# Kernel tuning notes

Measured on AMD Instinct MI355X. Metric: run time of the kernel, lower is better.

The kernel has to match this reference:

```python
import jax, jax.numpy as jnp
import numpy as np

B, T, C, H = 4, 2048, 1024, 16


def setup_inputs() -> dict:
    key = jax.random.key(0)
    k1, k2, k3 = jax.random.split(key, 3)
    x = jax.random.normal(k1, (B, T, C), dtype=jnp.float32)
    W_qkv = jax.random.normal(k2, (C, 3 * C), dtype=jnp.float32) * 0.02
    W_proj = jax.random.normal(k3, (C, C), dtype=jnp.float32) * 0.02
    return {"x": x, "W_qkv": W_qkv, "W_proj": W_proj}


def reference(x, W_qkv, W_proj):
    Bc, Tc, Cc = x.shape
    D = Cc // H
    qkv = x @ W_qkv                          # [B,T,3C]
    k, q, v = jnp.split(qkv, 3, axis=-1)     # split order k,q,v as in source
    q = q.reshape(Bc, Tc, H, D)
    k = k.reshape(Bc, Tc, H, D)
    v = v.reshape(Bc, Tc, H, D)
    # NOTE: module scales by full C**-0.5, not head_dim**-0.5
    scale = jnp.asarray(Cc, x.dtype) ** -0.5
    wei = jnp.einsum("bqhd,bkhd->bhqk", q, k) * scale      # [B,H,T,T]
    causal = jnp.tril(jnp.ones((Tc, Tc), dtype=bool))
    wei = jnp.where(causal[None, None], wei, jnp.asarray(-jnp.inf, x.dtype))
    att = jax.nn.softmax(wei, axis=-1)
    out = jnp.einsum("bhqk,bkhd->bqhd", att, v).reshape(Bc, Tc, Cc)
    return out @ W_proj
```

## Files before the change

kernel.cpp:

```cpp
#include <hip/hip_runtime.h>
#include <hip/hip_bf16.h>

#define B_   4
#define T_   2048
#define C_   1024
#define H_   16
#define D_   64
#define NQKV 3072
#define M_   (B_*T_)

typedef __attribute__((ext_vector_type(8))) short bf16x8;
typedef __attribute__((ext_vector_type(4))) short bf16x4;
typedef __attribute__((ext_vector_type(4))) float f32x4;
typedef __hip_bfloat16 bf16;

__device__ inline short f2bs(float f) {
    bf16 h = __float2bfloat16(f);
    return *(short*)&h;
}

__device__ inline void async_ld16(const bf16* g, bf16* l) {
    __builtin_amdgcn_global_load_lds(
        (const __attribute__((address_space(1))) void*)g,
        (__attribute__((address_space(3))) void*)l, 16, 0, 0);
}

__global__ __launch_bounds__(256) void prep(const float* __restrict__ x,
                                            const float* __restrict__ Wqkv,
                                            const float* __restrict__ Wproj,
                                            bf16* __restrict__ xb,
                                            bf16* __restrict__ wqkv_t,
                                            bf16* __restrict__ wproj_t) {
    __shared__ short t[32][33];
    const int bid = blockIdx.x;
    if (bid < 4096) {
        const long i = ((long)bid * 256 + threadIdx.x) * 8;
        const float4 a = *(const float4*)(x + i);
        const float4 bq = *(const float4*)(x + i + 4);
        bf16x8 o;
        o[0] = f2bs(a.x); o[1] = f2bs(a.y); o[2] = f2bs(a.z); o[3] = f2bs(a.w);
        o[4] = f2bs(bq.x); o[5] = f2bs(bq.y); o[6] = f2bs(bq.z); o[7] = f2bs(bq.w);
        *(bf16x8*)(xb + i) = o;
        return;
    }
    const float* in;  bf16* out;  int R, Ccol, r0, c0;
    if (bid < 7168) {
        const int b2 = bid - 4096;
        in = Wqkv; out = wqkv_t; R = C_; Ccol = NQKV;
        c0 = (b2 % 96) * 32; r0 = (b2 / 96) * 32;
    } else {
        const int b3 = bid - 7168;
        in = Wproj; out = wproj_t; R = C_; Ccol = C_;
        c0 = (b3 % 32) * 32; r0 = (b3 / 32) * 32;
    }
    const int xx = threadIdx.x & 31, yy = threadIdx.x >> 5;
#pragma unroll
    for (int i = 0; i < 4; i++)
        t[yy + 8*i][xx] = f2bs(in[(long)(r0 + yy + 8*i) * Ccol + c0 + xx]);
    __syncthreads();
#pragma unroll
    for (int i = 0; i < 4; i++)
        ((short*)out)[(long)(c0 + yy + 8*i) * R + r0 + xx] = t[xx][yy + 8*i];
}

__global__ __launch_bounds__(256) void transpose_v(const bf16* __restrict__ in,
                                                   bf16* __restrict__ out) {
    __shared__ short t[32][33];
    const int x = threadIdx.x & 31, y = threadIdx.x >> 5;
    const int t0 = blockIdx.x * 32, d0 = blockIdx.y * 32;
    const long base = (long)blockIdx.z * T_ * D_;
#pragma unroll
    for (int i = 0; i < 4; i++)
        t[y + 8*i][x] = ((const short*)in)[base + (long)(t0 + y + 8*i) * D_ + d0 + x];
    __syncthreads();
#pragma unroll
    for (int i = 0; i < 4; i++)
        ((short*)out)[base + (long)(d0 + y + 8*i) * T_ + t0 + x] = t[x][y + 8*i];
}

template<int MODE>
__global__ __launch_bounds__(256) void gemm_bt(const bf16* __restrict__ A,
                                               const bf16* __restrict__ Bt,
                                               float* __restrict__ outp,
                                               bf16* __restrict__ qb,
                                               bf16* __restrict__ kb,
                                               bf16* __restrict__ vb,
                                               int K, int N) {
    __shared__ __align__(16) bf16 As[128 * 32];
    __shared__ __align__(16) bf16 Bs[128 * 32];
    const int tid  = threadIdx.x;
    const int w    = tid >> 6, lane = tid & 63;
    const int g    = lane >> 4, ln = lane & 15;
    const int m0   = blockIdx.y * 128, n0 = blockIdx.x * 128;
    const int wm   = w & 1, wn = w >> 1;
    const int srow = lane >> 2;
    const int scol = (lane & 3) * 8;

    f32x4 acc[4][4] = {};

    for (int k0 = 0; k0 < K; k0 += 32) {
#pragma unroll
        for (int i = 0; i < 2; i++) {
            const int r = w * 32 + i * 16 + srow;
            async_ld16(A  + (long)(m0 + r) * K + k0 + scol, &As[r * 32 + scol]);
            async_ld16(Bt + (long)(n0 + r) * K + k0 + scol, &Bs[r * 32 + scol]);
        }
        __syncthreads();

        bf16x8 af[4], bfr[4];
#pragma unroll
        for (int i = 0; i < 4; i++)
            af[i]  = *(const bf16x8*)&As[(wm * 64 + i * 16 + ln) * 32 + g * 8];
#pragma unroll
        for (int j = 0; j < 4; j++)
            bfr[j] = *(const bf16x8*)&Bs[(wn * 64 + j * 16 + ln) * 32 + g * 8];
#pragma unroll
        for (int i = 0; i < 4; i++)
#pragma unroll
            for (int j = 0; j < 4; j++)
                acc[i][j] = __builtin_amdgcn_mfma_f32_16x16x32_bf16(af[i], bfr[j], acc[i][j], 0, 0, 0);
        __syncthreads();
    }

#pragma unroll
    for (int i = 0; i < 4; i++) {
#pragma unroll
        for (int j = 0; j < 4; j++) {
#pragma unroll
            for (int r = 0; r < 4; r++) {
                const int row = m0 + wm * 64 + i * 16 + g * 4 + r;
                const int col = n0 + wn * 64 + j * 16 + ln;
                if (MODE == 1) {
                    outp[(long)row * N + col] = acc[i][j][r];
                } else {
                    const int b = row >> 11, t = row & (T_ - 1);
                    const int seg = col >> 10;
                    const int c = col & (C_ - 1), h = c >> 6, d = c & 63;
                    if (seg == 0)
                        kb[(((long)(b * H_ + h)) * T_ + t) * D_ + d] = __float2bfloat16(acc[i][j][r]);
                    else if (seg == 1)
                        qb[(((long)(b * H_ + h)) * T_ + t) * D_ + d] = __float2bfloat16(acc[i][j][r] * 0.03125f);
                    else
                        vb[(((long)(b * H_ + h)) * T_ + t) * D_ + d] = __float2bfloat16(acc[i][j][r]);
                }
            }
        }
    }
}

__device__ inline void subtile(const bf16x8& qf0, const bf16x8& qf1,
                               f32x4* o, f32x4& l,
                               const short* Ks, const short* Vs, short* myP,
                               int q0, int kbase, int h2, int w, int g, int ln,
                               const bf16x8& ones) {
    f32x4 s[4] = {};
#pragma unroll
    for (int kj = 0; kj < 4; kj++) {
        const int krow = h2 * 64 + kj * 16 + ln;
        const bf16x8 kf0 = *(const bf16x8*)&Ks[krow * 64 + ((0 + g) ^ (krow & 7)) * 8];
        s[kj] = __builtin_amdgcn_mfma_f32_16x16x32_bf16(qf0, kf0, s[kj], 0, 0, 0);
        const bf16x8 kf1 = *(const bf16x8*)&Ks[krow * 64 + ((4 + g) ^ (krow & 7)) * 8];
        s[kj] = __builtin_amdgcn_mfma_f32_16x16x32_bf16(qf1, kf1, s[kj], 0, 0, 0);
    }
    const int rowg = q0 + w * 16 + g * 4;
    if (kbase == q0) {
#pragma unroll
        for (int kj = 0; kj < 4; kj++) {
            const int key = kbase + kj * 16 + ln;
#pragma unroll
            for (int r = 0; r < 4; r++) {
                float p = __expf(s[kj][r]);
                p = (key <= rowg + r) ? p : 0.f;
                const int prow = g * 4 + r;
                const int pc8 = (kj * 2 + (ln >> 3)) ^ (prow & 7);
                myP[prow * 64 + pc8 * 8 + (ln & 7)] = f2bs(p);
            }
        }
    } else {
#pragma unroll
        for (int kj = 0; kj < 4; kj++) {
#pragma unroll
            for (int r = 0; r < 4; r++) {
                const int prow = g * 4 + r;
                const int pc8 = (kj * 2 + (ln >> 3)) ^ (prow & 7);
                myP[prow * 64 + pc8 * 8 + (ln & 7)] = f2bs(__expf(s[kj][r]));
            }
        }
    }
    asm volatile("s_waitcnt lgkmcnt(0)" ::: "memory");
    const bf16x8 pf0 = *(const bf16x8*)&myP[ln * 64 + ((0 + g) ^ (ln & 7)) * 8];
    const bf16x8 pf1 = *(const bf16x8*)&myP[ln * 64 + ((4 + g) ^ (ln & 7)) * 8];
    l = __builtin_amdgcn_mfma_f32_16x16x32_bf16(ones, pf0, l, 0, 0, 0);
    l = __builtin_amdgcn_mfma_f32_16x16x32_bf16(ones, pf1, l, 0, 0, 0);
#pragma unroll
    for (int nb = 0; nb < 4; nb++) {
        const int drow = nb * 16 + ln;
        const bf16x8 vf0 = *(const bf16x8*)&Vs[drow * 128 + ((h2 * 8 + 0 + g) ^ (drow & 7)) * 8];
        o[nb] = __builtin_amdgcn_mfma_f32_16x16x32_bf16(vf0, pf0, o[nb], 0, 0, 0);
        const bf16x8 vf1 = *(const bf16x8*)&Vs[drow * 128 + ((h2 * 8 + 4 + g) ^ (drow & 7)) * 8];
        o[nb] = __builtin_amdgcn_mfma_f32_16x16x32_bf16(vf1, pf1, o[nb], 0, 0, 0);
    }
}

__global__ __launch_bounds__(256, 4) void flash(const bf16* __restrict__ qb,
                                                const bf16* __restrict__ kb,
                                                const bf16* __restrict__ vbT,
                                                bf16* __restrict__ att) {
    __shared__ __align__(16) short Ks[128 * 64];
    __shared__ __align__(16) short Vs[64 * 128];
    __shared__ __align__(16) short Ps[4 * 16 * 64];
    const int tid = threadIdx.x, w = tid >> 6, lane = tid & 63;
    const int g = lane >> 4, ln = lane & 15;
    const int lin = blockIdx.x;
    const int bh = lin & 63, p = lin >> 6;
    const int b = bh >> 4, h = bh & 15;
    const int q0A = p * 64, q0B = (31 - p) * 64;

    const bf16* qpA = qb + ((long)bh * T_ + q0A + w * 16 + ln) * D_;
    const bf16* qpB = qb + ((long)bh * T_ + q0B + w * 16 + ln) * D_;
    const bf16x8 qfA0 = *(const bf16x8*)(qpA + g * 8);
    const bf16x8 qfA1 = *(const bf16x8*)(qpA + 32 + g * 8);
    const bf16x8 qfB0 = *(const bf16x8*)(qpB + g * 8);
    const bf16x8 qfB1 = *(const bf16x8*)(qpB + 32 + g * 8);

    bf16x8 ones;
#pragma unroll
    for (int i = 0; i < 8; i++) ones[i] = 0x3F80;

    f32x4 oA[4] = {}, oB[4] = {};
    f32x4 lA = {}, lB = {};
    short* myP = &Ps[w * 16 * 64];

    const int nstB = (q0B + 64 + 127) >> 7;
    for (int s = 0; s < nstB; s++) {
        const int k0 = s * 128;
        bf16x8 kr[4], vr[4];
#pragma unroll
        for (int i = 0; i < 4; i++) {
            const int cc = i * 256 + tid;
            kr[i] = *(const bf16x8*)&kb [((long)bh * T_ + k0 + (cc >> 3)) * D_ + (cc & 7) * 8];
            vr[i] = *(const bf16x8*)&vbT[((long)bh * D_ + (cc >> 4)) * T_ + k0 + (cc & 15) * 8];
        }
        __syncthreads();
#pragma unroll
        for (int i = 0; i < 4; i++) {
            const int cc = i * 256 + tid;
            const int key = cc >> 3, c8 = cc & 7;
            *(bf16x8*)&Ks[key * 64 + (c8 ^ (key & 7)) * 8] = kr[i];
            const int d = cc >> 4, c16 = cc & 15;
            *(bf16x8*)&Vs[d * 128 + (c16 ^ (d & 7)) * 8] = vr[i];
        }
        __syncthreads();

#pragma unroll
        for (int h2 = 0; h2 < 2; h2++) {
            const int kbase = k0 + h2 * 64;
            if (kbase <= q0A + 63)
                subtile(qfA0, qfA1, oA, lA, Ks, Vs, myP, q0A, kbase, h2, w, g, ln, ones);
            if (kbase <= q0B + 63)
                subtile(qfB0, qfB1, oB, lB, Ks, Vs, myP, q0B, kbase, h2, w, g, ln, ones);
        }
    }

#pragma unroll
    for (int ti = 0; ti < 2; ti++) {
        const f32x4* o = ti ? oB : oA;
        const float invl = 1.f / (ti ? lB[0] : lA[0]);
        const int q = (ti ? q0B : q0A) + w * 16 + ln;
#pragma unroll
        for (int nb = 0; nb < 4; nb++) {
            bf16x4 pk;
#pragma unroll
            for (int r = 0; r < 4; r++) pk[r] = f2bs(o[nb][r] * invl);
            *(bf16x4*)&att[((long)b * T_ + q) * C_ + h * D_ + nb * 16 + g * 4] = pk;
        }
    }
}

extern "C" void kernel_launch(void* const* d_in, const int* in_sizes, int n_in,
                              void* d_out, int out_size, void* d_ws, size_t ws_size,
                              hipStream_t stream) {
    const float* x     = (const float*)d_in[0];
    const float* Wqkv  = (const float*)d_in[1];
    const float* Wproj = (const float*)d_in[2];
    float* out = (float*)d_out;

    char* ws = (char*)d_ws;
    bf16* wqkv_t  = (bf16*)(ws);
    bf16* wproj_t = (bf16*)(ws + 6291456);
    bf16* qb      = (bf16*)(ws + 8388608);
    bf16* kb      = (bf16*)(ws + 25165824);
    bf16* vb0     = (bf16*)(ws + 41943040);
    bf16* xb      = (bf16*)(ws + 58720256);
    bf16* vbT     = xb;
    bf16* att     = vb0;
    (void)ws_size; (void)in_sizes; (void)n_in; (void)out_size;

    prep<<<dim3(8192), dim3(256), 0, stream>>>(x, Wqkv, Wproj, xb, wqkv_t, wproj_t);
    gemm_bt<0><<<dim3(NQKV / 128, M_ / 128), dim3(256), 0, stream>>>(
        xb, wqkv_t, (float*)nullptr, qb, kb, vb0, C_, NQKV);
    transpose_v<<<dim3(T_ / 32, D_ / 32, B_ * H_), dim3(256), 0, stream>>>(vb0, vbT);
    flash<<<dim3(1024), dim3(256), 0, stream>>>(qb, kb, vbT, att);
    gemm_bt<1><<<dim3(C_ / 128, M_ / 128), dim3(256), 0, stream>>>(
        att, wproj_t, out, (bf16*)nullptr, (bf16*)nullptr, (bf16*)nullptr, C_, C_);
}
```

Before: 279.1 us.

## Fuse V transpose into QKV GEMM epilogue and widen GEMM K-tile with swizzle

```diff
diff --git a/kernel.cpp b/kernel.cpp
--- a/kernel.cpp
+++ b/kernel.cpp
@@ -19,7 +19,7 @@
     return *(short*)&h;
 }
 
-__device__ inline void async_ld16(const bf16* g, bf16* l) {
+__device__ inline void async_ld16(const bf16* g, const short* l) {
     __builtin_amdgcn_global_load_lds(
         (const __attribute__((address_space(1))) void*)g,
         (__attribute__((address_space(3))) void*)l, 16, 0, 0);
@@ -63,63 +63,77 @@
         ((short*)out)[(long)(c0 + yy + 8*i) * R + r0 + xx] = t[xx][yy + 8*i];
 }
 
-__global__ __launch_bounds__(256) void transpose_v(const bf16* __restrict__ in,
-                                                   bf16* __restrict__ out) {
-    __shared__ short t[32][33];
-    const int x = threadIdx.x & 31, y = threadIdx.x >> 5;
-    const int t0 = blockIdx.x * 32, d0 = blockIdx.y * 32;
-    const long base = (long)blockIdx.z * T_ * D_;
-#pragma unroll
-    for (int i = 0; i < 4; i++)
-        t[y + 8*i][x] = ((const short*)in)[base + (long)(t0 + y + 8*i) * D_ + d0 + x];
-    __syncthreads();
-#pragma unroll
-    for (int i = 0; i < 4; i++)
-        ((short*)out)[base + (long)(d0 + y + 8*i) * T_ + t0 + x] = t[x][y + 8*i];
-}
-
 template<int MODE>
 __global__ __launch_bounds__(256) void gemm_bt(const bf16* __restrict__ A,
                                                const bf16* __restrict__ Bt,
                                                float* __restrict__ outp,
                                                bf16* __restrict__ qb,
                                                bf16* __restrict__ kb,
-                                               bf16* __restrict__ vb,
+                                               bf16* __restrict__ vbT,
                                                int K, int N) {
-    __shared__ __align__(16) bf16 As[128 * 32];
-    __shared__ __align__(16) bf16 Bs[128 * 32];
+    __shared__ __align__(16) short SMEM[18432];
+    short* As = SMEM;
+    short* Bs = SMEM + 8192;
     const int tid  = threadIdx.x;
     const int w    = tid >> 6, lane = tid & 63;
     const int g    = lane >> 4, ln = lane & 15;
     const int m0   = blockIdx.y * 128, n0 = blockIdx.x * 128;
     const int wm   = w & 1, wn = w >> 1;
-    const int srow = lane >> 2;
-    const int scol = (lane & 3) * 8;
 
     f32x4 acc[4][4] = {};
 
-    for (int k0 = 0; k0 < K; k0 += 32) {
-#pragma unroll
-        for (int i = 0; i < 2; i++) {
-            const int r = w * 32 + i * 16 + srow;
-            async_ld16(A  + (long)(m0 + r) * K + k0 + scol, &As[r * 32 + scol]);
-            async_ld16(Bt + (long)(n0 + r) * K + k0 + scol, &Bs[r * 32 + scol]);
-        }
-        __syncthreads();
-
-        bf16x8 af[4], bfr[4];
+    for (int k0 = 0; k0 < K; k0 += 64) {
+#pragma unroll
+        for (int i = 0; i < 4; i++) {
+            const int s   = w * 256 + i * 64 + lane;
+            const int row = s >> 3, c8 = (s & 7) ^ ((s >> 3) & 7);
+            async_ld16(A  + (long)(m0 + row) * K + k0 + c8 * 8, &As[s * 8]);
+            async_ld16(Bt + (long)(n0 + row) * K + k0 + c8 * 8, &Bs[s * 8]);
+        }
+        __syncthreads();
+
+#pragma unroll
+        for (int kh = 0; kh < 2; kh++) {
+            bf16x8 af[4], bfr[4];
+#pragma unroll
+            for (int i = 0; i < 4; i++)
+                af[i]  = *(const bf16x8*)&As[(wm * 64 + i * 16 + ln) * 64 + ((kh * 4 + g) ^ (ln & 7)) * 8];
+#pragma unroll
+            for (int j = 0; j < 4; j++)
+                bfr[j] = *(const bf16x8*)&Bs[(wn * 64 + j * 16 + ln) * 64 + ((kh * 4 + g) ^ (ln & 7)) * 8];
+#pragma unroll
+            for (int i = 0; i < 4; i++)
+#pragma unroll
+                for (int j = 0; j < 4; j++)
+                    acc[i][j] = __builtin_amdgcn_mfma_f32_16x16x32_bf16(af[i], bfr[j], acc[i][j], 0, 0, 0);
+        }
+        __syncthreads();
+    }
+
+    if (MODE == 0 && n0 >= 2048) {
+        short* Vt = SMEM;
 #pragma unroll
         for (int i = 0; i < 4; i++)
-            af[i]  = *(const bf16x8*)&As[(wm * 64 + i * 16 + ln) * 32 + g * 8];
-#pragma unroll
-        for (int j = 0; j < 4; j++)
-            bfr[j] = *(const bf16x8*)&Bs[(wn * 64 + j * 16 + ln) * 32 + g * 8];
-#pragma unroll
-        for (int i = 0; i < 4; i++)
 #pragma unroll
             for (int j = 0; j < 4; j++)
-                acc[i][j] = __builtin_amdgcn_mfma_f32_16x16x32_bf16(af[i], bfr[j], acc[i][j], 0, 0, 0);
-        __syncthreads();
+#pragma unroll
+                for (int r = 0; r < 4; r++) {
+                    const int tl = wm * 64 + i * 16 + g * 4 + r;
+                    const int dl = wn * 64 + j * 16 + ln;
+                    Vt[dl * 144 + tl] = f2bs(acc[i][j][r]);
+                }
+        __syncthreads();
+        const int b  = m0 >> 11, tb = m0 & (T_ - 1);
+        const int h0 = (n0 - 2048) >> 6;
+#pragma unroll
+        for (int ii = 0; ii < 8; ii++) {
+            const int s = ii * 256 + tid;
+            const int dl = s >> 4, t16 = s & 15;
+            const bf16x8 v = *(const bf16x8*)&Vt[dl * 144 + t16 * 8];
+            const int h = h0 + (dl >> 6), d = dl & 63;
+            *(bf16x8*)&vbT[(((long)(b * H_ + h)) * D_ + d) * T_ + tb + t16 * 8] = v;
+        }
+        return;
     }
 
 #pragma unroll
@@ -138,10 +152,8 @@
                     const int c = col & (C_ - 1), h = c >> 6, d = c & 63;
                     if (seg == 0)
                         kb[(((long)(b * H_ + h)) * T_ + t) * D_ + d] = __float2bfloat16(acc[i][j][r]);
-                    else if (seg == 1)
+                    else
                         qb[(((long)(b * H_ + h)) * T_ + t) * D_ + d] = __float2bfloat16(acc[i][j][r] * 0.03125f);
-                    else
-                        vb[(((long)(b * H_ + h)) * T_ + t) * D_ + d] = __float2bfloat16(acc[i][j][r]);
                 }
             }
         }
@@ -290,16 +302,14 @@
     bf16* wproj_t = (bf16*)(ws + 6291456);
     bf16* qb      = (bf16*)(ws + 8388608);
     bf16* kb      = (bf16*)(ws + 25165824);
-    bf16* vb0     = (bf16*)(ws + 41943040);
+    bf16* vbT     = (bf16*)(ws + 41943040);
     bf16* xb      = (bf16*)(ws + 58720256);
-    bf16* vbT     = xb;
-    bf16* att     = vb0;
+    bf16* att     = xb;
     (void)ws_size; (void)in_sizes; (void)n_in; (void)out_size;
 
     prep<<<dim3(8192), dim3(256), 0, stream>>>(x, Wqkv, Wproj, xb, wqkv_t, wproj_t);
     gemm_bt<0><<<dim3(NQKV / 128, M_ / 128), dim3(256), 0, stream>>>(
-        xb, wqkv_t, (float*)nullptr, qb, kb, vb0, C_, NQKV);
-    transpose_v<<<dim3(T_ / 32, D_ / 32, B_ * H_), dim3(256), 0, stream>>>(vb0, vbT);
+        xb, wqkv_t, (float*)nullptr, qb, kb, vbT, C_, NQKV);
     flash<<<dim3(1024), dim3(256), 0, stream>>>(qb, kb, vbT, att);
     gemm_bt<1><<<dim3(C_ / 128, M_ / 128), dim3(256), 0, stream>>>(
         att, wproj_t, out, (bf16*)nullptr, (bf16*)nullptr, (bf16*)nullptr, C_, C_);
```

New measurement: 248.3 us. -11.0%, faster.
